# Kernel optimization log

Measured on AMD Instinct MI355X. Metric: run time of the kernel, lower is better.

## Reference

```python
import jax, jax.numpy as jnp
import numpy as np

T, B, D, H = 2048, 4, 1024, 16
HD = D // H  # head_dim = 64


def setup_inputs() -> dict:
    key = jax.random.key(0)
    ks = jax.random.split(key, 12)
    s = 1.0 / np.sqrt(D)
    return {
        "query": jax.random.normal(ks[0], (T, B, D), jnp.float32),
        "key": jax.random.normal(ks[1], (T, B, D), jnp.float32),
        "value": jax.random.normal(ks[2], (T, B, D), jnp.float32),
        "time_decay": jax.random.uniform(ks[3], (T, B, D), jnp.float32),
        "Wq": jax.random.normal(ks[4], (D, D), jnp.float32) * s,
        "bq": jax.random.normal(ks[5], (D,), jnp.float32) * s,
        "Wk": jax.random.normal(ks[6], (D, D), jnp.float32) * s,
        "bk": jax.random.normal(ks[7], (D,), jnp.float32) * s,
        "Wv": jax.random.normal(ks[8], (D, D), jnp.float32) * s,
        "bv": jax.random.normal(ks[9], (D,), jnp.float32) * s,
        "Wo": jax.random.normal(ks[10], (D, D), jnp.float32) * s,
        "bo": jax.random.normal(ks[11], (D,), jnp.float32) * s,
    }


def reference(query, key, value, time_decay, Wq, bq, Wk, bk, Wv, bv, Wo, bo):
    # Linear projections (torch Linear: x @ W.T + b). Inputs are (T, B, D).
    def split_heads(x, W, b):
        y = x @ W.T + b  # (T, B, D)
        # -> (B, H, T, HD)
        return y.reshape(T, B, H, HD).transpose(1, 2, 0, 3)

    Q = split_heads(query, Wq, bq)
    K = split_heads(key, Wk, bk)
    V = split_heads(value, Wv, bv)

    scale = 1.0 / np.sqrt(HD)
    scores = jnp.einsum("bhqd,bhkd->bhqk", Q, K) * scale  # (B, H, T, T)
    attn = jax.nn.softmax(scores, axis=-1)
    ctx = jnp.einsum("bhqk,bhkd->bhqd", attn, V)  # (B, H, T, HD)
    # -> (T, B, D)
    ctx = ctx.transpose(2, 0, 1, 3).reshape(T, B, D)
    out = ctx @ Wo.T + bo
    return out * time_decay
```

## Files before the change

kernel.cpp:

```cpp
#include <hip/hip_runtime.h>

#define TT 2048
#define BB 4
#define DD 1024
#define HH 16
#define HDIM 64
#define MM (TT*BB)

typedef __attribute__((ext_vector_type(4))) float float4v;
typedef _Float16 half8 __attribute__((ext_vector_type(8)));
typedef _Float16 half4 __attribute__((ext_vector_type(4)));
typedef _Float16 half2v __attribute__((ext_vector_type(2)));

static __device__ __forceinline__ half4 pk4(float a, float b, float c, float d) {
    half2v h0 = __builtin_bit_cast(half2v, __builtin_amdgcn_cvt_pkrtz(a, b));
    half2v h1 = __builtin_bit_cast(half2v, __builtin_amdgcn_cvt_pkrtz(c, d));
    half4 hv; hv[0]=h0[0]; hv[1]=h0[1]; hv[2]=h1[0]; hv[3]=h1[1];
    return hv;
}

static __device__ __forceinline__ float fexp2(float x) {
    float r; asm("v_exp_f32 %0, %1" : "=v"(r) : "v"(x)); return r;
}

#define GLD16(g, l) __builtin_amdgcn_global_load_lds( \
    (const __attribute__((address_space(1))) unsigned int*)(g), \
    (__attribute__((address_space(3))) unsigned int*)(l), 16, 0, 0)

__global__ __launch_bounds__(256) void cvt_f16(
    const float* __restrict__ q, const float* __restrict__ k, const float* __restrict__ v,
    const float* __restrict__ wq, const float* __restrict__ wk, const float* __restrict__ wv,
    const float* __restrict__ wo,
    _Float16* __restrict__ qh, _Float16* __restrict__ kh, _Float16* __restrict__ vh,
    _Float16* __restrict__ wqh, _Float16* __restrict__ wkh, _Float16* __restrict__ wvh,
    _Float16* __restrict__ woh)
{
    const int z = blockIdx.z;
    const float* src; _Float16* dst; int n;
    switch (z) {
        case 0: src=q;  dst=qh;  n=MM*DD/8; break;
        case 1: src=k;  dst=kh;  n=MM*DD/8; break;
        case 2: src=v;  dst=vh;  n=MM*DD/8; break;
        case 3: src=wq; dst=wqh; n=DD*DD/8; break;
        case 4: src=wk; dst=wkh; n=DD*DD/8; break;
        case 5: src=wv; dst=wvh; n=DD*DD/8; break;
        default: src=wo; dst=woh; n=DD*DD/8; break;
    }
    for (int c = blockIdx.x*blockDim.x + threadIdx.x; c < n; c += gridDim.x*blockDim.x) {
        const float4v* s4 = (const float4v*)src + (size_t)c*2;
        float4v a = s4[0], b = s4[1];
        *(half4*)(dst + (size_t)c*8)     = pk4(a[0],a[1],a[2],a[3]);
        *(half4*)(dst + (size_t)c*8 + 4) = pk4(b[0],b[1],b[2],b[3]);
    }
}

__global__ __launch_bounds__(256, 4) void qkv_gemm(
    const _Float16* __restrict__ xq, const _Float16* __restrict__ xk, const _Float16* __restrict__ xv,
    const _Float16* __restrict__ wall,
    const float* __restrict__ bq, const float* __restrict__ bk, const float* __restrict__ bv,
    _Float16* __restrict__ dq, _Float16* __restrict__ dk, _Float16* __restrict__ dv)
{
    __shared__ __attribute__((aligned(16))) _Float16 As0[128*32], As1[128*32];
    __shared__ __attribute__((aligned(16))) _Float16 Bs0[128*32], Bs1[128*32];

    const int id   = blockIdx.x;
    const int wgid = (id & 7)*192 + (id >> 3);
    const int z    = wgid / 512;
    const int rem  = wgid & 511;
    const int by   = rem >> 3, bx = rem & 7;
    const int m0   = by*128, n0l = bx*128;

    const _Float16* X = (z==0)?xq:((z==1)?xk:xv);
    const float* Bb   = (z==0)?bq:((z==1)?bk:bv);
    _Float16* Dst     = (z==0)?dq:((z==1)?dk:dv);
    const float osc   = (z==0) ? 0.18033688011112042f : 1.0f;

    const int tid=threadIdx.x, lane=tid&63, w=tid>>6;
    const int wm=w>>1, wn=w&1;
    const int lrow=lane&15, lg=lane>>4;
    const int swA = (lg ^ (lrow&3))*8;

    const int gsl = ((lane&3) ^ ((lane>>2)&3))*8;
    const _Float16* ga = X    + (size_t)(m0 + w*32 + (lane>>2))*DD + gsl;
    const _Float16* gb = wall + (size_t)(z*1024 + n0l + w*32 + (lane>>2))*DD + gsl;

    float4v acc[4][4];
    for (int i=0;i<4;i++) for (int j=0;j<4;j++) acc[i][j]=(float4v){0.f,0.f,0.f,0.f};

    GLD16(ga,                 As0 + (w*32)*32);
    GLD16(ga + (size_t)16*DD, As0 + (w*32+16)*32);
    GLD16(gb,                 Bs0 + (w*32)*32);
    GLD16(gb + (size_t)16*DD, Bs0 + (w*32+16)*32);
    __syncthreads();

#define QSTEP(T, CA, CB_, NA, NB_, PREF)                                      \
    {                                                                         \
        if (PREF) {                                                           \
            const size_t kk = (size_t)((T)+1)*32;                             \
            GLD16(ga + kk,                 NA + (w*32)*32);                   \
            GLD16(ga + (size_t)16*DD + kk, NA + (w*32+16)*32);                \
            GLD16(gb + kk,                 NB_ + (w*32)*32);                  \
            GLD16(gb + (size_t)16*DD + kk, NB_ + (w*32+16)*32);               \
        }                                                                     \
        half8 a[4], b[4];                                                     \
        _Pragma("unroll")                                                     \
        for (int i=0;i<4;i++) a[i] = *(const half8*)&CA[(wm*64+i*16+lrow)*32 + swA];  \
        _Pragma("unroll")                                                     \
        for (int j=0;j<4;j++) b[j] = *(const half8*)&CB_[(wn*64+j*16+lrow)*32 + swA]; \
        _Pragma("unroll")                                                     \
        for (int i=0;i<4;i++)                                                 \
        _Pragma("unroll")                                                     \
        for (int j=0;j<4;j++)                                                 \
            acc[i][j] = __builtin_amdgcn_mfma_f32_16x16x32_f16(a[i], b[j], acc[i][j],0,0,0); \
        __syncthreads();                                                      \
    }

    for (int t=0; t<32; t+=2) {
        QSTEP(t,   As0, Bs0, As1, Bs1, 1);
        QSTEP(t+1, As1, Bs1, As0, Bs0, (t+2)<32);
    }
#undef QSTEP

    #pragma unroll
    for (int j=0;j<4;j++) {
        int n = n0l + wn*64 + j*16 + lrow;
        float bias = Bb[n];
        int h = n >> 6, hd = n & 63;
        #pragma unroll
        for (int i=0;i<4;i++)
        #pragma unroll
        for (int r=0;r<4;r++) {
            int m = m0 + wm*64 + i*16 + lg*4 + r;
            int tt = m >> 2, b = m & 3;
            Dst[((size_t)(b*HH + h)*TT + tt)*HDIM + hd] = (_Float16)((acc[i][j][r] + bias)*osc);
        }
    }
}

__global__ __launch_bounds__(256) void v_transpose(
    const _Float16* __restrict__ Vb, _Float16* __restrict__ VbT)
{
    const int tile = blockIdx.x;
    const int bh   = blockIdx.y;
    const int tid = threadIdx.x, tg = tid & 15, hg = tid >> 4;
    const int t0 = tile*64;

    half4 rv[4];
    #pragma unroll
    for (int r=0;r<4;r++)
        rv[r] = *(const half4*)(Vb + ((size_t)bh*TT + t0 + tg*4 + r)*HDIM + hg*4);
    #pragma unroll
    for (int c=0;c<4;c++) {
        half4 tv; tv[0]=rv[0][c]; tv[1]=rv[1][c]; tv[2]=rv[2][c]; tv[3]=rv[3][c];
        *(half4*)(VbT + ((size_t)bh*HDIM + hg*4 + c)*TT + t0 + tg*4) = tv;
    }
}

__global__ __launch_bounds__(256, 4) void attn(
    const _Float16* __restrict__ Qg, const _Float16* __restrict__ Kg,
    const _Float16* __restrict__ VT, _Float16* __restrict__ Ctx)
{
    __shared__ __attribute__((aligned(16))) _Float16 Kt0[64*64], Kt1[64*64];
    __shared__ __attribute__((aligned(16))) _Float16 Vs0[64*64], Vs1[64*64];

    const int id = blockIdx.x;
    const int bh = id & 63, qt = id >> 6;
    const int b = bh >> 4, h = bh & 15;
    const int tid = threadIdx.x, lane = tid & 63, w = tid >> 6;
    const int lrow = lane & 15, lg = lane >> 4;

    const _Float16* Qb  = Qg + ((size_t)bh*TT + qt*128)*HDIM;
    const _Float16* Kb  = Kg + (size_t)bh*TT*HDIM;
    const _Float16* Vtb = VT + (size_t)bh*HDIM*TT;

    const int srow = w*16 + (lane>>3);
    const int scol = ((lane&7) ^ (lane>>3))*8;

    half8 qf[2][2];
    #pragma unroll
    for (int i=0;i<2;i++)
    #pragma unroll
    for (int kc=0;kc<2;kc++)
        qf[i][kc] = *(const half8*)(Qb + (size_t)(w*32 + i*16 + lrow)*HDIM + kc*32 + lg*8);

    float4v oacc[2][4];
    for (int i=0;i<2;i++) for (int j=0;j<4;j++) oacc[i][j]=(float4v){0.f,0.f,0.f,0.f};
    float lsum[2] = {0.f, 0.f};

    #pragma unroll
    for (int s=0;s<2;s++) {
        GLD16(Kb  + (size_t)(srow + s*8)*HDIM + scol, Kt0 + (w*16 + s*8)*64);
        GLD16(Vtb + (size_t)(srow + s*8)*TT   + scol, Vs0 + (w*16 + s*8)*64);
    }
    __syncthreads();

    const int swz = (lrow & 7) << 3;

#define ASTEP(KT, CK, CV, NK, NV, PREF)                                       \
    {                                                                         \
        if (PREF) {                                                           \
            _Pragma("unroll")                                                 \
            for (int s=0;s<2;s++) {                                           \
                GLD16(Kb  + (size_t)(((KT)+1)*64 + srow + s*8)*HDIM + scol, NK + (w*16 + s*8)*64); \
                GLD16(Vtb + (size_t)(srow + s*8)*TT + ((KT)+1)*64 + scol,   NV + (w*16 + s*8)*64); \
            }                                                                 \
        }                                                                     \
        float4v st[4][2];                                                     \
        _Pragma("unroll")                                                     \
        for (int j=0;j<4;j++) for (int i=0;i<2;i++) st[j][i]=(float4v){0.f,0.f,0.f,0.f}; \
        _Pragma("unroll")                                                     \
        for (int kc=0;kc<2;kc++) {                                            \
            half8 kf[4];                                                      \
            _Pragma("unroll")                                                 \
            for (int j=0;j<4;j++)                                             \
                kf[j] = *(const half8*)&CK[(j*16 + lrow)*64 + ((kc*32 + lg*8) ^ swz)]; \
            __builtin_amdgcn_s_setprio(1);                                    \
            _Pragma("unroll")                                                 \
            for (int j=0;j<4;j++)                                             \
            _Pragma("unroll")                                                 \
            for (int i=0;i<2;i++)                                             \
                st[j][i] = __builtin_amdgcn_mfma_f32_16x16x32_f16(kf[j], qf[i][kc], st[j][i],0,0,0); \
            __builtin_amdgcn_s_setprio(0);                                    \
        }                                                                     \
        _Pragma("unroll")                                                     \
        for (int j=0;j<4;j++) {                                               \
            half4 pa[2];                                                      \
            _Pragma("unroll")                                                 \
            for (int i=0;i<2;i++) {                                           \
                float p0 = fexp2(st[j][i][0]);                                \
                float p1 = fexp2(st[j][i][1]);                                \
                float p2 = fexp2(st[j][i][2]);                                \
                float p3 = fexp2(st[j][i][3]);                                \
                lsum[i] += (p0+p1)+(p2+p3);                                   \
                pa[i] = pk4(p0,p1,p2,p3);                                     \
            }                                                                 \
            half4 vf[4];                                                      \
            _Pragma("unroll")                                                 \
            for (int jo=0;jo<4;jo++)                                          \
                vf[jo] = *(const half4*)&CV[(jo*16 + lrow)*64 + ((j*16 + lg*4) ^ swz)]; \
            __builtin_amdgcn_s_setprio(1);                                    \
            _Pragma("unroll")                                                 \
            for (int i=0;i<2;i++)                                             \
            _Pragma("unroll")                                                 \
            for (int jo=0;jo<4;jo++)                                          \
                oacc[i][jo] = __builtin_amdgcn_mfma_f32_16x16x16f16(vf[jo], pa[i], oacc[i][jo],0,0,0); \
            __builtin_amdgcn_s_setprio(0);                                    \
        }                                                                     \
        __syncthreads();                                                      \
    }

    for (int kt = 0; kt < 32; kt += 2) {
        ASTEP(kt,   Kt0, Vs0, Kt1, Vs1, 1);
        ASTEP(kt+1, Kt1, Vs1, Kt0, Vs0, (kt+2)<32);
    }
#undef ASTEP

    #pragma unroll
    for (int i=0;i<2;i++) {
        float s = lsum[i];
        s += __shfl_xor(s, 16, 64);
        s += __shfl_xor(s, 32, 64);
        lsum[i] = s;
    }

    #pragma unroll
    for (int i=0;i<2;i++) {
        float inv = 1.f / lsum[i];
        int t = qt*128 + w*32 + i*16 + lrow;
        _Float16* crow = Ctx + ((size_t)t*BB + b)*DD + h*HDIM;
        #pragma unroll
        for (int jo=0;jo<4;jo++) {
            *(half4*)(crow + jo*16 + lg*4) =
                pk4(oacc[i][jo][0]*inv, oacc[i][jo][1]*inv,
                    oacc[i][jo][2]*inv, oacc[i][jo][3]*inv);
        }
    }
}

__global__ __launch_bounds__(256, 4) void out_gemm(
    const _Float16* __restrict__ Cx, const _Float16* __restrict__ Woh,
    const float* __restrict__ bo, const float* __restrict__ td,
    float* __restrict__ Out)
{
    __shared__ __attribute__((aligned(16))) _Float16 As0[128*32], As1[128*32];
    __shared__ __attribute__((aligned(16))) _Float16 Bs0[128*32], Bs1[128*32];

    const int id   = blockIdx.x;
    const int wgid = (id & 7)*64 + (id >> 3);
    const int by   = wgid >> 3, bx = wgid & 7;
    const int m0   = by*128, n0 = bx*128;

    const int tid=threadIdx.x, lane=tid&63, w=tid>>6;
    const int wm=w>>1, wn=w&1;
    const int lrow=lane&15, lg=lane>>4;
    const int swA = (lg ^ (lrow&3))*8;

    const int gsl = ((lane&3) ^ ((lane>>2)&3))*8;
    const _Float16* ga = Cx  + (size_t)(m0 + w*32 + (lane>>2))*DD + gsl;
    const _Float16* gb = Woh + (size_t)(n0 + w*32 + (lane>>2))*DD + gsl;

    float4v acc[4][4];
    for (int i=0;i<4;i++) for (int j=0;j<4;j++) acc[i][j]=(float4v){0.f,0.f,0.f,0.f};

    GLD16(ga,                 As0 + (w*32)*32);
    GLD16(ga + (size_t)16*DD, As0 + (w*32+16)*32);
    GLD16(gb,                 Bs0 + (w*32)*32);
    GLD16(gb + (size_t)16*DD, Bs0 + (w*32+16)*32);
    __syncthreads();

#define OSTEP(T, CA, CB_, NA, NB_, PREF)                                      \
    {                                                                         \
        if (PREF) {                                                           \
            const size_t kk = (size_t)((T)+1)*32;                             \
            GLD16(ga + kk,                 NA + (w*32)*32);                   \
            GLD16(ga + (size_t)16*DD + kk, NA + (w*32+16)*32);                \
            GLD16(gb + kk,                 NB_ + (w*32)*32);                  \
            GLD16(gb + (size_t)16*DD + kk, NB_ + (w*32+16)*32);               \
        }                                                                     \
        half8 a[4], b[4];                                                     \
        _Pragma("unroll")                                                     \
        for (int i=0;i<4;i++) a[i] = *(const half8*)&CA[(wm*64+i*16+lrow)*32 + swA];  \
        _Pragma("unroll")                                                     \
        for (int j=0;j<4;j++) b[j] = *(const half8*)&CB_[(wn*64+j*16+lrow)*32 + swA]; \
        _Pragma("unroll")                                                     \
        for (int i=0;i<4;i++)                                                 \
        _Pragma("unroll")                                                     \
        for (int j=0;j<4;j++)                                                 \
            acc[i][j] = __builtin_amdgcn_mfma_f32_16x16x32_f16(a[i], b[j], acc[i][j],0,0,0); \
        __syncthreads();                                                      \
    }

    for (int t=0; t<32; t+=2) {
        OSTEP(t,   As0, Bs0, As1, Bs1, 1);
        OSTEP(t+1, As1, Bs1, As0, Bs0, (t+2)<32);
    }
#undef OSTEP

    #pragma unroll
    for (int j=0;j<4;j++) {
        int n = n0 + wn*64 + j*16 + lrow;
        float bias = bo[n];
        #pragma unroll
        for (int i=0;i<4;i++)
        #pragma unroll
        for (int r=0;r<4;r++) {
            int m = m0 + wm*64 + i*16 + lg*4 + r;
            size_t off = (size_t)m*DD + n;
            Out[off] = (acc[i][j][r] + bias) * td[off];
        }
    }
}

extern "C" void kernel_launch(void* const* d_in, const int* in_sizes, int n_in,
                              void* d_out, int out_size, void* d_ws, size_t ws_size,
                              hipStream_t stream) {
    const float* q  = (const float*)d_in[0];
    const float* k  = (const float*)d_in[1];
    const float* v  = (const float*)d_in[2];
    const float* td = (const float*)d_in[3];
    const float* Wq = (const float*)d_in[4];
    const float* bq = (const float*)d_in[5];
    const float* Wk = (const float*)d_in[6];
    const float* bk = (const float*)d_in[7];
    const float* Wv = (const float*)d_in[8];
    const float* bv = (const float*)d_in[9];
    const float* Wo = (const float*)d_in[10];
    const float* bo = (const float*)d_in[11];
    float* out = (float*)d_out;

    _Float16* qh  = (_Float16*)d_ws;
    _Float16* kh  = qh  + (size_t)MM*DD;
    _Float16* vh  = kh  + (size_t)MM*DD;
    _Float16* wqh = vh  + (size_t)MM*DD;
    _Float16* wkh = wqh + (size_t)DD*DD;
    _Float16* wvh = wkh + (size_t)DD*DD;
    _Float16* woh = wvh + (size_t)DD*DD;
    _Float16* Qb  = woh + (size_t)DD*DD;
    _Float16* Kb  = Qb  + (size_t)MM*DD;
    _Float16* Vb  = Kb  + (size_t)MM*DD;
    _Float16* VbT = vh;
    _Float16* Cx  = qh;

    cvt_f16    <<<dim3(2048,1,7), 256, 0, stream>>>(q,k,v, Wq,Wk,Wv,Wo, qh,kh,vh, wqh,wkh,wvh,woh);
    qkv_gemm   <<<dim3(1536),     256, 0, stream>>>(qh,kh,vh, wqh, bq,bk,bv, Qb,Kb,Vb);
    v_transpose<<<dim3(32,64),    256, 0, stream>>>(Vb, VbT);
    attn       <<<dim3(1024),     256, 0, stream>>>(Qb, Kb, VbT, Cx);
    out_gemm   <<<dim3(512),      256, 0, stream>>>(Cx, woh, bo, td, out);
}
```

Before: 389.6 us.

## Deepen GEMM K-tiles, use explicit vmcnt waits, fuse V transpose into QKV epilogue

Both GEMMs move to 64-wide K tiles with a new XOR swizzle, which halves the number of barriers per K loop. In the GEMMs and the attention kernel, __syncthreads is replaced by raw s_barrier plus explicit s_waitcnt vmcnt, so the next tile's prefetch can stay in flight while the current tile is computed. The V-projection epilogue writes V directly in transposed layout, which removes the separate v_transpose kernel and its extra pass over V. The launch-bounds occupancy hints are dropped and the cvt grid is shrunk; larger LDS tiles may lower occupancy, and the transposed V store is strided and poorly coalesced.

```diff
diff --git a/kernel.cpp b/kernel.cpp
--- a/kernel.cpp
+++ b/kernel.cpp
@@ -26,6 +26,9 @@
 #define GLD16(g, l) __builtin_amdgcn_global_load_lds( \
     (const __attribute__((address_space(1))) unsigned int*)(g), \
     (__attribute__((address_space(3))) unsigned int*)(l), 16, 0, 0)
+
+#define BAR()    __builtin_amdgcn_s_barrier()
+#define VMCNT(N) asm volatile("s_waitcnt vmcnt(" #N ")" ::: "memory")
 
 __global__ __launch_bounds__(256) void cvt_f16(
     const float* __restrict__ q, const float* __restrict__ k, const float* __restrict__ v,
@@ -54,14 +57,14 @@
     }
 }
 
-__global__ __launch_bounds__(256, 4) void qkv_gemm(
+__global__ __launch_bounds__(256) void qkv_gemm(
     const _Float16* __restrict__ xq, const _Float16* __restrict__ xk, const _Float16* __restrict__ xv,
     const _Float16* __restrict__ wall,
     const float* __restrict__ bq, const float* __restrict__ bk, const float* __restrict__ bv,
     _Float16* __restrict__ dq, _Float16* __restrict__ dk, _Float16* __restrict__ dv)
 {
-    __shared__ __attribute__((aligned(16))) _Float16 As0[128*32], As1[128*32];
-    __shared__ __attribute__((aligned(16))) _Float16 Bs0[128*32], Bs1[128*32];
+    __shared__ __attribute__((aligned(16))) _Float16 As0[128*64], As1[128*64];
+    __shared__ __attribute__((aligned(16))) _Float16 Bs0[128*64], Bs1[128*64];
 
     const int id   = blockIdx.x;
     const int wgid = (id & 7)*192 + (id >> 3);
@@ -78,81 +81,95 @@
     const int tid=threadIdx.x, lane=tid&63, w=tid>>6;
     const int wm=w>>1, wn=w&1;
     const int lrow=lane&15, lg=lane>>4;
-    const int swA = (lg ^ (lrow&3))*8;
-
-    const int gsl = ((lane&3) ^ ((lane>>2)&3))*8;
-    const _Float16* ga = X    + (size_t)(m0 + w*32 + (lane>>2))*DD + gsl;
-    const _Float16* gb = wall + (size_t)(z*1024 + n0l + w*32 + (lane>>2))*DD + gsl;
+    const int swzr = (lrow & 7) << 3;
+
+    const int scol = ((lane&7) ^ (lane>>3))*8;
+    const _Float16* ga = X    + (size_t)(m0 + w*32 + (lane>>3))*DD + scol;
+    const _Float16* gb = wall + (size_t)(z*1024 + n0l + w*32 + (lane>>3))*DD + scol;
 
     float4v acc[4][4];
     for (int i=0;i<4;i++) for (int j=0;j<4;j++) acc[i][j]=(float4v){0.f,0.f,0.f,0.f};
 
-    GLD16(ga,                 As0 + (w*32)*32);
-    GLD16(ga + (size_t)16*DD, As0 + (w*32+16)*32);
-    GLD16(gb,                 Bs0 + (w*32)*32);
-    GLD16(gb + (size_t)16*DD, Bs0 + (w*32+16)*32);
-    __syncthreads();
+    #pragma unroll
+    for (int s=0;s<4;s++) GLD16(ga + (size_t)s*8*DD, As0 + (w*32+s*8)*64);
+    #pragma unroll
+    for (int s=0;s<4;s++) GLD16(gb + (size_t)s*8*DD, Bs0 + (w*32+s*8)*64);
+    VMCNT(0);
+    BAR();
 
 #define QSTEP(T, CA, CB_, NA, NB_, PREF)                                      \
     {                                                                         \
+        BAR();   \
         if (PREF) {                                                           \
-            const size_t kk = (size_t)((T)+1)*32;                             \
-            GLD16(ga + kk,                 NA + (w*32)*32);                   \
-            GLD16(ga + (size_t)16*DD + kk, NA + (w*32+16)*32);                \
-            GLD16(gb + kk,                 NB_ + (w*32)*32);                  \
-            GLD16(gb + (size_t)16*DD + kk, NB_ + (w*32+16)*32);               \
+            const size_t kk = (size_t)((T)+1)*64;                             \
+            _Pragma("unroll")                                                 \
+            for (int s=0;s<4;s++) GLD16(ga + (size_t)s*8*DD + kk, NA + (w*32+s*8)*64);  \
+            _Pragma("unroll")                                                 \
+            for (int s=0;s<4;s++) GLD16(gb + (size_t)s*8*DD + kk, NB_ + (w*32+s*8)*64); \
+            VMCNT(8);    \
+        } else {                                                              \
+            VMCNT(0);                                                         \
         }                                                                     \
+        BAR();                             \
         half8 a[4], b[4];                                                     \
         _Pragma("unroll")                                                     \
-        for (int i=0;i<4;i++) a[i] = *(const half8*)&CA[(wm*64+i*16+lrow)*32 + swA];  \
-        _Pragma("unroll")                                                     \
-        for (int j=0;j<4;j++) b[j] = *(const half8*)&CB_[(wn*64+j*16+lrow)*32 + swA]; \
+        for (int i=0;i<4;i++) a[i] = *(const half8*)&CA[(wm*64+i*16+lrow)*64 + ((0*32+lg*8) ^ swzr)];  \
+        _Pragma("unroll")                                                     \
+        for (int j=0;j<4;j++) b[j] = *(const half8*)&CB_[(wn*64+j*16+lrow)*64 + ((0*32+lg*8) ^ swzr)]; \
         _Pragma("unroll")                                                     \
         for (int i=0;i<4;i++)                                                 \
         _Pragma("unroll")                                                     \
         for (int j=0;j<4;j++)                                                 \
             acc[i][j] = __builtin_amdgcn_mfma_f32_16x16x32_f16(a[i], b[j], acc[i][j],0,0,0); \
-        __syncthreads();                                                      \
-    }
-
-    for (int t=0; t<32; t+=2) {
+        _Pragma("unroll")                                                     \
+        for (int i=0;i<4;i++) a[i] = *(const half8*)&CA[(wm*64+i*16+lrow)*64 + ((1*32+lg*8) ^ swzr)];  \
+        _Pragma("unroll")                                                     \
+        for (int j=0;j<4;j++) b[j] = *(const half8*)&CB_[(wn*64+j*16+lrow)*64 + ((1*32+lg*8) ^ swzr)]; \
+        _Pragma("unroll")                                                     \
+        for (int i=0;i<4;i++)                                                 \
+        _Pragma("unroll")                                                     \
+        for (int j=0;j<4;j++)                                                 \
+            acc[i][j] = __builtin_amdgcn_mfma_f32_16x16x32_f16(a[i], b[j], acc[i][j],0,0,0); \
+    }
+
+    for (int t=0; t<14; t+=2) {
         QSTEP(t,   As0, Bs0, As1, Bs1, 1);
-        QSTEP(t+1, As1, Bs1, As0, Bs0, (t+2)<32);
-    }
+        QSTEP(t+1, As1, Bs1, As0, Bs0, 1);
+    }
+    QSTEP(14, As0, Bs0, As1, Bs1, 1);
+    QSTEP(15, As1, Bs1, As0, Bs0, 0);
 #undef QSTEP
 
-    #pragma unroll
-    for (int j=0;j<4;j++) {
-        int n = n0l + wn*64 + j*16 + lrow;
-        float bias = Bb[n];
-        int h = n >> 6, hd = n & 63;
+    if (z == 2) {
         #pragma unroll
-        for (int i=0;i<4;i++)
+        for (int j=0;j<4;j++) {
+            int n = n0l + wn*64 + j*16 + lrow;
+            float bias = Bb[n];
+            int h = n >> 6, hd = n & 63;
+            #pragma unroll
+            for (int i=0;i<4;i++)
+            #pragma unroll
+            for (int r=0;r<4;r++) {
+                int m = m0 + wm*64 + i*16 + lg*4 + r;
+                int tt = m >> 2, b = m & 3;
+                Dst[((size_t)(b*HH + h)*HDIM + hd)*TT + tt] = (_Float16)(acc[i][j][r] + bias);
+            }
+        }
+    } else {
         #pragma unroll
-        for (int r=0;r<4;r++) {
-            int m = m0 + wm*64 + i*16 + lg*4 + r;
-            int tt = m >> 2, b = m & 3;
-            Dst[((size_t)(b*HH + h)*TT + tt)*HDIM + hd] = (_Float16)((acc[i][j][r] + bias)*osc);
+        for (int j=0;j<4;j++) {
+            int n = n0l + wn*64 + j*16 + lrow;
+            float bias = Bb[n];
+            int h = n >> 6, hd = n & 63;
+            #pragma unroll
+            for (int i=0;i<4;i++)
+            #pragma unroll
+            for (int r=0;r<4;r++) {
+                int m = m0 + wm*64 + i*16 + lg*4 + r;
+                int tt = m >> 2, b = m & 3;
+                Dst[((size_t)(b*HH + h)*TT + tt)*HDIM + hd] = (_Float16)((acc[i][j][r] + bias)*osc);
+            }
         }
-    }
-}
-
-__global__ __launch_bounds__(256) void v_transpose(
-    const _Float16* __restrict__ Vb, _Float16* __restrict__ VbT)
-{
-    const int tile = blockIdx.x;
-    const int bh   = blockIdx.y;
-    const int tid = threadIdx.x, tg = tid & 15, hg = tid >> 4;
-    const int t0 = tile*64;
-
-    half4 rv[4];
-    #pragma unroll
-    for (int r=0;r<4;r++)
-        rv[r] = *(const half4*)(Vb + ((size_t)bh*TT + t0 + tg*4 + r)*HDIM + hg*4);
-    #pragma unroll
-    for (int c=0;c<4;c++) {
-        half4 tv; tv[0]=rv[0][c]; tv[1]=rv[1][c]; tv[2]=rv[2][c]; tv[3]=rv[3][c];
-        *(half4*)(VbT + ((size_t)bh*HDIM + hg*4 + c)*TT + t0 + tg*4) = tv;
     }
 }
 
@@ -192,19 +209,25 @@
         GLD16(Kb  + (size_t)(srow + s*8)*HDIM + scol, Kt0 + (w*16 + s*8)*64);
         GLD16(Vtb + (size_t)(srow + s*8)*TT   + scol, Vs0 + (w*16 + s*8)*64);
     }
-    __syncthreads();
+    VMCNT(0);
+    BAR();
 
     const int swz = (lrow & 7) << 3;
 
 #define ASTEP(KT, CK, CV, NK, NV, PREF)                                       \
     {                                                                         \
+        BAR();                  \
         if (PREF) {                                                           \
             _Pragma("unroll")                                                 \
             for (int s=0;s<2;s++) {                                           \
                 GLD16(Kb  + (size_t)(((KT)+1)*64 + srow + s*8)*HDIM + scol, NK + (w*16 + s*8)*64); \
                 GLD16(Vtb + (size_t)(srow + s*8)*TT + ((KT)+1)*64 + scol,   NV + (w*16 + s*8)*64); \
             }                                                                 \
+            VMCNT(4);                                                         \
+        } else {                                                              \
+            VMCNT(0);                                                         \
         }                                                                     \
+        BAR();                              \
         float4v st[4][2];                                                     \
         _Pragma("unroll")                                                     \
         for (int j=0;j<4;j++) for (int i=0;i<2;i++) st[j][i]=(float4v){0.f,0.f,0.f,0.f}; \
@@ -246,13 +269,14 @@
                 oacc[i][jo] = __builtin_amdgcn_mfma_f32_16x16x16f16(vf[jo], pa[i], oacc[i][jo],0,0,0); \
             __builtin_amdgcn_s_setprio(0);                                    \
         }                                                                     \
-        __syncthreads();                                                      \
-    }
-
-    for (int kt = 0; kt < 32; kt += 2) {
+    }
+
+    for (int kt = 0; kt < 30; kt += 2) {
         ASTEP(kt,   Kt0, Vs0, Kt1, Vs1, 1);
-        ASTEP(kt+1, Kt1, Vs1, Kt0, Vs0, (kt+2)<32);
-    }
+        ASTEP(kt+1, Kt1, Vs1, Kt0, Vs0, 1);
+    }
+    ASTEP(30, Kt0, Vs0, Kt1, Vs1, 1);
+    ASTEP(31, Kt1, Vs1, Kt0, Vs0, 0);
 #undef ASTEP
 
     #pragma unroll
@@ -277,13 +301,13 @@
     }
 }
 
-__global__ __launch_bounds__(256, 4) void out_gemm(
+__global__ __launch_bounds__(256) void out_gemm(
     const _Float16* __restrict__ Cx, const _Float16* __restrict__ Woh,
     const float* __restrict__ bo, const float* __restrict__ td,
     float* __restrict__ Out)
 {
-    __shared__ __attribute__((aligned(16))) _Float16 As0[128*32], As1[128*32];
-    __shared__ __attribute__((aligned(16))) _Float16 Bs0[128*32], Bs1[128*32];
+    __shared__ __attribute__((aligned(16))) _Float16 As0[128*64], As1[128*64];
+    __shared__ __attribute__((aligned(16))) _Float16 Bs0[128*64], Bs1[128*64];
 
     const int id   = blockIdx.x;
     const int wgid = (id & 7)*64 + (id >> 3);
@@ -293,47 +317,63 @@
     const int tid=threadIdx.x, lane=tid&63, w=tid>>6;
     const int wm=w>>1, wn=w&1;
     const int lrow=lane&15, lg=lane>>4;
-    const int swA = (lg ^ (lrow&3))*8;
-
-    const int gsl = ((lane&3) ^ ((lane>>2)&3))*8;
-    const _Float16* ga = Cx  + (size_t)(m0 + w*32 + (lane>>2))*DD + gsl;
-    const _Float16* gb = Woh + (size_t)(n0 + w*32 + (lane>>2))*DD + gsl;
+    const int swzr = (lrow & 7) << 3;
+
+    const int scol = ((lane&7) ^ (lane>>3))*8;
+    const _Float16* ga = Cx  + (size_t)(m0 + w*32 + (lane>>3))*DD + scol;
+    const _Float16* gb = Woh + (size_t)(n0 + w*32 + (lane>>3))*DD + scol;
 
     float4v acc[4][4];
     for (int i=0;i<4;i++) for (int j=0;j<4;j++) acc[i][j]=(float4v){0.f,0.f,0.f,0.f};
 
-    GLD16(ga,                 As0 + (w*32)*32);
-    GLD16(ga + (size_t)16*DD, As0 + (w*32+16)*32);
-    GLD16(gb,                 Bs0 + (w*32)*32);
-    GLD16(gb + (size_t)16*DD, Bs0 + (w*32+16)*32);
-    __syncthreads();
+    #pragma unroll
+    for (int s=0;s<4;s++) GLD16(ga + (size_t)s*8*DD, As0 + (w*32+s*8)*64);
+    #pragma unroll
+    for (int s=0;s<4;s++) GLD16(gb + (size_t)s*8*DD, Bs0 + (w*32+s*8)*64);
+    VMCNT(0);
+    BAR();
 
 #define OSTEP(T, CA, CB_, NA, NB_, PREF)                                      \
     {                                                                         \
+        BAR();                                                                \
         if (PREF) {                                                           \
-            const size_t kk = (size_t)((T)+1)*32;                             \
-            GLD16(ga + kk,                 NA + (w*32)*32);                   \
-            GLD16(ga + (size_t)16*DD + kk, NA + (w*32+16)*32);                \
-            GLD16(gb + kk,                 NB_ + (w*32)*32);                  \
-            GLD16(gb + (size_t)16*DD + kk, NB_ + (w*32+16)*32);               \
+            const size_t kk = (size_t)((T)+1)*64;                             \
+            _Pragma("unroll")                                                 \
+            for (int s=0;s<4;s++) GLD16(ga + (size_t)s*8*DD + kk, NA + (w*32+s*8)*64);  \
+            _Pragma("unroll")                                                 \
+            for (int s=0;s<4;s++) GLD16(gb + (size_t)s*8*DD + kk, NB_ + (w*32+s*8)*64); \
+            VMCNT(8);                                                         \
+        } else {                                                              \
+            VMCNT(0);                                                         \
         }                                                                     \
+        BAR();                                                                \
         half8 a[4], b[4];                                                     \
         _Pragma("unroll")                                                     \
-        for (int i=0;i<4;i++) a[i] = *(const half8*)&CA[(wm*64+i*16+lrow)*32 + swA];  \
-        _Pragma("unroll")                                                     \
-        for (int j=0;j<4;j++) b[j] = *(const half8*)&CB_[(wn*64+j*16+lrow)*32 + swA]; \
+        for (int i=0;i<4;i++) a[i] = *(const half8*)&CA[(wm*64+i*16+lrow)*64 + ((0*32+lg*8) ^ swzr)];  \
+        _Pragma("unroll")                                                     \
+        for (int j=0;j<4;j++) b[j] = *(const half8*)&CB_[(wn*64+j*16+lrow)*64 + ((0*32+lg*8) ^ swzr)]; \
         _Pragma("unroll")                                                     \
         for (int i=0;i<4;i++)                                                 \
         _Pragma("unroll")                                                     \
         for (int j=0;j<4;j++)                                                 \
             acc[i][j] = __builtin_amdgcn_mfma_f32_16x16x32_f16(a[i], b[j], acc[i][j],0,0,0); \
-        __syncthreads();                                                      \
-    }
-
-    for (int t=0; t<32; t+=2) {
+        _Pragma("unroll")                                                     \
+        for (int i=0;i<4;i++) a[i] = *(const half8*)&CA[(wm*64+i*16+lrow)*64 + ((1*32+lg*8) ^ swzr)];  \
+        _Pragma("unroll")                                                     \
+        for (int j=0;j<4;j++) b[j] = *(const half8*)&CB_[(wn*64+j*16+lrow)*64 + ((1*32+lg*8) ^ swzr)]; \
+        _Pragma("unroll")                                                     \
+        for (int i=0;i<4;i++)                                                 \
+        _Pragma("unroll")                                                     \
+        for (int j=0;j<4;j++)                                                 \
+            acc[i][j] = __builtin_amdgcn_mfma_f32_16x16x32_f16(a[i], b[j], acc[i][j],0,0,0); \
+    }
+
+    for (int t=0; t<14; t+=2) {
         OSTEP(t,   As0, Bs0, As1, Bs1, 1);
-        OSTEP(t+1, As1, Bs1, As0, Bs0, (t+2)<32);
-    }
+        OSTEP(t+1, As1, Bs1, As0, Bs0, 1);
+    }
+    OSTEP(14, As0, Bs0, As1, Bs1, 1);
+    OSTEP(15, As1, Bs1, As0, Bs0, 0);
 #undef OSTEP
 
     #pragma unroll
@@ -377,13 +417,11 @@
     _Float16* woh = wvh + (size_t)DD*DD;
     _Float16* Qb  = woh + (size_t)DD*DD;
     _Float16* Kb  = Qb  + (size_t)MM*DD;
-    _Float16* Vb  = Kb  + (size_t)MM*DD;
-    _Float16* VbT = vh;
+    _Float16* VbT = Kb  + (size_t)MM*DD;
     _Float16* Cx  = qh;
 
-    cvt_f16    <<<dim3(2048,1,7), 256, 0, stream>>>(q,k,v, Wq,Wk,Wv,Wo, qh,kh,vh, wqh,wkh,wvh,woh);
-    qkv_gemm   <<<dim3(1536),     256, 0, stream>>>(qh,kh,vh, wqh, bq,bk,bv, Qb,Kb,Vb);
-    v_transpose<<<dim3(32,64),    256, 0, stream>>>(Vb, VbT);
-    attn       <<<dim3(1024),     256, 0, stream>>>(Qb, Kb, VbT, Cx);
-    out_gemm   <<<dim3(512),      256, 0, stream>>>(Cx, woh, bo, td, out);
-}
+    cvt_f16 <<<dim3(512,1,7), 256, 0, stream>>>(q,k,v, Wq,Wk,Wv,Wo, qh,kh,vh, wqh,wkh,wvh,woh);
+    qkv_gemm<<<dim3(1536),    256, 0, stream>>>(qh,kh,vh, wqh, bq,bk,bv, Qb,Kb,VbT);
+    attn    <<<dim3(1024),    256, 0, stream>>>(Qb, Kb, VbT, Cx);
+    out_gemm<<<dim3(512),     256, 0, stream>>>(Cx, woh, bo, td, out);
+}
```

Result: slower. 453.5 us (+16.4%).
